# Kernel optimization log

Measured on AMD Instinct MI355X. Metric: run time of the kernel, lower is better.

The kernel has to match this reference:

```python
import jax, jax.numpy as jnp
import numpy as np

NHEAD = 8
K_NEIGH = 16


def setup_inputs() -> dict:
    key = jax.random.key(0)
    ks = jax.random.split(key, 6)
    B, L, D = 4, 4096, 512
    x = jax.random.normal(ks[0], (B, L, D), dtype=jnp.float32)
    positions = jax.random.uniform(ks[1], (B, L, 3), dtype=jnp.float32)
    in_proj_w = jax.random.normal(ks[2], (3 * D, D), dtype=jnp.float32) * 0.02
    in_proj_b = jax.random.normal(ks[3], (3 * D,), dtype=jnp.float32) * 0.02
    out_proj_w = jax.random.normal(ks[4], (D, D), dtype=jnp.float32) * 0.02
    out_proj_b = jax.random.normal(ks[5], (D,), dtype=jnp.float32) * 0.02
    return {"x": x, "positions": positions, "in_proj_w": in_proj_w,
            "in_proj_b": in_proj_b, "out_proj_w": out_proj_w, "out_proj_b": out_proj_b}


def _sparse_attention(x, positions, in_proj_w, in_proj_b, out_proj_w, out_proj_b):
    B, L, D = x.shape
    H, dh = NHEAD, D // NHEAD
    K = min(K_NEIGH, L)
    scale = 1.0 / jnp.sqrt(jnp.asarray(dh, x.dtype))

    # Pairwise distances [B, L, L]; topk smallest -> neighbor indices [B, L, K].
    diff = positions[:, :, None, :] - positions[:, None, :, :]
    dist = jnp.sqrt(jnp.sum(diff * diff, axis=-1))
    _, nbr = jax.lax.top_k(-dist, K)  # [B, L, K]

    Wq, Wk, Wv = in_proj_w[:D], in_proj_w[D:2 * D], in_proj_w[2 * D:]
    bq, bk, bv = in_proj_b[:D], in_proj_b[D:2 * D], in_proj_b[2 * D:]

    # Query is x[b, i] itself (self is always its own nearest neighbor at dist 0),
    # so the selected attention row equals attention with query x[b, i] over neighbors.
    q = ((x @ Wq.T + bq) * scale).reshape(B, L, H, dh)

    # Gather neighbor features: [B, L, K, D]
    b_idx = jnp.arange(B)[:, None, None]
    local_x = x[b_idx, nbr]
    k = (local_x @ Wk.T + bk).reshape(B, L, K, H, dh)
    v = (local_x @ Wv.T + bv).reshape(B, L, K, H, dh)

    scores = jnp.einsum('blhd,blkhd->blhk', q, k)
    attn = jax.nn.softmax(scores, axis=-1)
    ctx = jnp.einsum('blhk,blkhd->blhd', attn, v).reshape(B, L, D)
    out = ctx @ out_proj_w.T + out_proj_b

    # Faithful fallback: if i not among its neighbors, pass through x[b, i].
    is_in = jnp.any(nbr == jnp.arange(L)[None, :, None], axis=-1)  # [B, L]
    return jnp.where(is_in[..., None], out, x)


def reference(x, positions, in_proj_w, in_proj_b, out_proj_w, out_proj_b):
    return _sparse_attention(x, positions, in_proj_w, in_proj_b, out_proj_w, out_proj_b)
```

## Files before the change

### kernel.cpp

```cpp
#include <hip/hip_runtime.h>
#include <cfloat>
#include <cmath>

constexpr int B = 4;
constexpr int L = 4096;
constexpr int D = 512;
constexpr int NH = 8;
constexpr int DH = 64;
constexpr int KN = 16;
constexpr int M = B * L;
constexpr int N_IN = 3 * D;
constexpr int NCELL = 512;

typedef __attribute__((ext_vector_type(8))) short short8;
typedef __attribute__((ext_vector_type(4))) float f32x4;
typedef unsigned short ushort;

__device__ __forceinline__ ushort f2bf(float f) {
  unsigned u = __float_as_uint(f);
  u = u + 0x7fffu + ((u >> 16) & 1u);
  return (ushort)(u >> 16);
}
__device__ __forceinline__ float bf2f(ushort h) {
  return __uint_as_float(((unsigned)h) << 16);
}
__device__ __forceinline__ float dot8(const uint4 qu, const uint4 ku, float a) {
  a = fmaf(bf2f((ushort)qu.x), bf2f((ushort)ku.x), a);
  a = fmaf(bf2f((ushort)(qu.x >> 16)), bf2f((ushort)(ku.x >> 16)), a);
  a = fmaf(bf2f((ushort)qu.y), bf2f((ushort)ku.y), a);
  a = fmaf(bf2f((ushort)(qu.y >> 16)), bf2f((ushort)(ku.y >> 16)), a);
  a = fmaf(bf2f((ushort)qu.z), bf2f((ushort)ku.z), a);
  a = fmaf(bf2f((ushort)(qu.z >> 16)), bf2f((ushort)(ku.z >> 16)), a);
  a = fmaf(bf2f((ushort)qu.w), bf2f((ushort)ku.w), a);
  a = fmaf(bf2f((ushort)(qu.w >> 16)), bf2f((ushort)(ku.w >> 16)), a);
  return a;
}
__device__ __forceinline__ void acc8(float wgt, const uint4 vv, float (&acc)[8]) {
  acc[0] = fmaf(wgt, bf2f((ushort)vv.x), acc[0]);
  acc[1] = fmaf(wgt, bf2f((ushort)(vv.x >> 16)), acc[1]);
  acc[2] = fmaf(wgt, bf2f((ushort)vv.y), acc[2]);
  acc[3] = fmaf(wgt, bf2f((ushort)(vv.y >> 16)), acc[3]);
  acc[4] = fmaf(wgt, bf2f((ushort)vv.z), acc[4]);
  acc[5] = fmaf(wgt, bf2f((ushort)(vv.z >> 16)), acc[5]);
  acc[6] = fmaf(wgt, bf2f((ushort)vv.w), acc[6]);
  acc[7] = fmaf(wgt, bf2f((ushort)(vv.w >> 16)), acc[7]);
}
__device__ __forceinline__ uint2 pack4hi(const float4 v) {
  uint2 o;
  o.x = (unsigned)f2bf(v.x) | ((unsigned)f2bf(v.y) << 16);
  o.y = (unsigned)f2bf(v.z) | ((unsigned)f2bf(v.w) << 16);
  return o;
}
__device__ __forceinline__ void gload16(const void* g, void* l) {
  __builtin_amdgcn_global_load_lds(
      (const __attribute__((address_space(1))) void*)g,
      (__attribute__((address_space(3))) void*)l, 16, 0, 0);
}
__device__ __forceinline__ int morton3(int x, int y, int z) {
  int m = 0;
#pragma unroll
  for (int i = 0; i < 3; ++i)
    m |= (((x >> i) & 1) << (3 * i + 2)) | (((y >> i) & 1) << (3 * i + 1)) |
         (((z >> i) & 1) << (3 * i));
  return m;
}

__global__ __launch_bounds__(256) void cvt_x_kernel(const float* __restrict__ in,
                                                    ushort* __restrict__ out) {
  const int n8 = M * D / 8;
  for (int i = blockIdx.x * 256 + threadIdx.x; i < n8; i += gridDim.x * 256) {
    const float4 v0 = reinterpret_cast<const float4*>(in)[i * 2];
    const float4 v1 = reinterpret_cast<const float4*>(in)[i * 2 + 1];
    uint4 o;
    const uint2 a = pack4hi(v0), b2 = pack4hi(v1);
    o.x = a.x; o.y = a.y; o.z = b2.x; o.w = b2.y;
    reinterpret_cast<uint4*>(out)[i] = o;
  }
}

__global__ __launch_bounds__(256) void cvt_w_kernel(const float* __restrict__ in_w,
                                                    const float* __restrict__ out_w,
                                                    ushort* __restrict__ iwh,
                                                    ushort* __restrict__ owh,
                                                    ushort* __restrict__ owl) {
  const int ni8 = N_IN * D / 8;
  const int no8 = D * D / 8;
  for (int i = blockIdx.x * 256 + threadIdx.x; i < ni8 + no8; i += gridDim.x * 256) {
    if (i < ni8) {
      const float4 v0 = reinterpret_cast<const float4*>(in_w)[i * 2];
      const float4 v1 = reinterpret_cast<const float4*>(in_w)[i * 2 + 1];
      uint4 o;
      const uint2 a = pack4hi(v0), b2 = pack4hi(v1);
      o.x = a.x; o.y = a.y; o.z = b2.x; o.w = b2.y;
      reinterpret_cast<uint4*>(iwh)[i] = o;
    } else {
      const int j = i - ni8;
      const float4 v0 = reinterpret_cast<const float4*>(out_w)[j * 2];
      const float4 v1 = reinterpret_cast<const float4*>(out_w)[j * 2 + 1];
      uint4 oh, ol;
      const uint2 a = pack4hi(v0), b2 = pack4hi(v1);
      oh.x = a.x; oh.y = a.y; oh.z = b2.x; oh.w = b2.y;
      const float4 r0 = make_float4(v0.x - bf2f(f2bf(v0.x)), v0.y - bf2f(f2bf(v0.y)),
                                    v0.z - bf2f(f2bf(v0.z)), v0.w - bf2f(f2bf(v0.w)));
      const float4 r1 = make_float4(v1.x - bf2f(f2bf(v1.x)), v1.y - bf2f(f2bf(v1.y)),
                                    v1.z - bf2f(f2bf(v1.z)), v1.w - bf2f(f2bf(v1.w)));
      const uint2 c = pack4hi(r0), d2 = pack4hi(r1);
      ol.x = c.x; ol.y = c.y; ol.z = d2.x; ol.w = d2.y;
      reinterpret_cast<uint4*>(owh)[j] = oh;
      reinterpret_cast<uint4*>(owl)[j] = ol;
    }
  }
}

__global__ __launch_bounds__(512) void sort_kernel(const float* __restrict__ pos,
                                                   int* __restrict__ qorder) {
  __shared__ int hist[NCELL];
  __shared__ int scanbuf[NCELL];
  const int b = blockIdx.x;
  const int t = threadIdx.x;
  hist[t] = 0;
  __syncthreads();

  int cells[8], ranks[8];
  const float* p = pos + (size_t)b * L * 3;
#pragma unroll
  for (int q = 0; q < 8; ++q) {
    const int i = q * 512 + t;
    const int ix = min(7, max(0, (int)(p[3 * i + 0] * 8.f)));
    const int iy = min(7, max(0, (int)(p[3 * i + 1] * 8.f)));
    const int iz = min(7, max(0, (int)(p[3 * i + 2] * 8.f)));
    cells[q] = morton3(ix, iy, iz);
    ranks[q] = atomicAdd(&hist[cells[q]], 1);
  }
  __syncthreads();

  int accv = hist[t];
  const int orig = accv;
  scanbuf[t] = accv;
  __syncthreads();
  for (int s = 1; s < NCELL; s <<= 1) {
    const int o = (t >= s) ? scanbuf[t - s] : 0;
    __syncthreads();
    accv += o;
    scanbuf[t] = accv;
    __syncthreads();
  }
  hist[t] = accv - orig;
  __syncthreads();

#pragma unroll
  for (int q = 0; q < 8; ++q) {
    const int i = q * 512 + t;
    qorder[b * L + hist[cells[q]] + ranks[q]] = i;
  }
}

constexpr int TP = 65;

__global__ __launch_bounds__(512) void topk_kernel(const float* __restrict__ pos,
                                                   int* __restrict__ nbr,
                                                   int* __restrict__ isin) {
  __shared__ float sxT[64 * TP], syT[64 * TP], szT[64 * TP];
  __shared__ unsigned long long lst[8 * 64];
  const int wave = threadIdx.x >> 6;
  const int lane = threadIdx.x & 63;
  const int b = blockIdx.x >> 9;
  const int l = (blockIdx.x & 511) * 8 + wave;
  const int row = b * L + l;

  const float* p = pos + (size_t)b * L * 3;
  for (int i = threadIdx.x; i < L; i += 512) {
    const int a = (i & 63) * TP + (i >> 6);
    sxT[a] = p[3 * i + 0];
    syT[a] = p[3 * i + 1];
    szT[a] = p[3 * i + 2];
  }
  __syncthreads();

  const int qa = (l & 63) * TP + (l >> 6);
  const float qx = sxT[qa], qy = syT[qa], qz = szT[qa];

  float mA = FLT_MAX, mB2 = FLT_MAX, mC = FLT_MAX, mD2 = FLT_MAX;
  const int base = lane * TP;
  for (int j = 0; j < 64; j += 4) {
#define D2(t, acc)                                                   \
    {                                                                \
      const int a = base + j + t;                                    \
      const float dx = qx - sxT[a], dy = qy - syT[a], dz = qz - szT[a]; \
      acc = fminf(acc, fmaf(dx, dx, fmaf(dy, dy, dz * dz)));         \
    }
    D2(0, mA) D2(1, mB2) D2(2, mC) D2(3, mD2)
#undef D2
  }
  const unsigned mbits = __float_as_uint(fminf(fminf(mA, mB2), fminf(mC, mD2)));

  unsigned lo = 1, hi = 0x40400001u;
  while (lo < hi) {
    const unsigned mid = (lo + hi) >> 1;
    const int c = __popcll(__ballot(mbits < mid));
    if (c >= 16) hi = mid; else lo = mid + 1;
  }
  const unsigned P = lo + 16;

  int cnt = 0;
  unsigned long long am = __ballot(mbits < P);
  const unsigned long long below = (1ull << lane) - 1ull;
  while (am) {
    const int pl = (int)__builtin_ctzll(am);
    am &= am - 1;
    const int a = pl * TP + lane;
    const float dx = qx - sxT[a], dy = qy - syT[a], dz = qz - szT[a];
    const float d2 = fmaf(dx, dx, fmaf(dy, dy, dz * dz));
    const bool hit = __float_as_uint(d2) < P;
    const unsigned long long msk = __ballot(hit);
    if (hit) {
      const int slot = cnt + __popcll(msk & below);
      if (slot < 64) {
        const unsigned c = (unsigned)(lane * 64 + pl);
        lst[wave * 64 + slot] =
            ((unsigned long long)__float_as_uint(sqrtf(d2)) << 32) | c;
      }
    }
    cnt += __popcll(msk);
  }
  const int n = min(cnt, 64);

  const unsigned long long mine = (lane < n) ? lst[wave * 64 + lane] : ~0ull;
  int r = 0;
  for (int i = 0; i < n; ++i) r += (lst[wave * 64 + i] < mine) ? 1 : 0;

  const int idx = (int)(unsigned)(mine & 0xffffffffu);
  const bool wr = (lane < n) && (r < 16);
  if (wr) nbr[(size_t)row * KN + r] = idx;
  const unsigned long long hit2 = __ballot(wr && idx == l);
  if (lane == 0) isin[row] = hit2 ? 1 : 0;
}

constexpr int BM = 128, BN = 128, BK = 32;
constexpr int BK2 = 64;

__global__ __launch_bounds__(256) void gemm_in(const ushort* __restrict__ A,
                                               const ushort* __restrict__ W,
                                               const float* __restrict__ bias,
                                               ushort* __restrict__ qb,
                                               ushort* __restrict__ kb,
                                               ushort* __restrict__ vb) {
  __shared__ ushort Ah[BM * BK2];
  __shared__ ushort Bh[BN * BK2];

  const int tid = threadIdx.x;
  const int m0 = blockIdx.x * BM;
  const int n0 = blockIdx.y * BN;

  const int wv = tid >> 6;
  const int lane = tid & 63;
  const int srow0 = wv * 8 + (lane >> 3);
  const int gchunk = (lane & 7) ^ (lane >> 3);
  const ushort* Asrc = A + (size_t)(m0 + srow0) * D + gchunk * 8;
  const ushort* Wsrc = W + (size_t)(n0 + srow0) * D + gchunk * 8;
  ushort* AhB0 = Ah + (wv * 8) * BK2;
  ushort* AhB1 = Ah + (wv * 8 + 32) * BK2;
  ushort* AhB2 = Ah + (wv * 8 + 64) * BK2;
  ushort* AhB3 = Ah + (wv * 8 + 96) * BK2;
  ushort* BhB0 = Bh + (wv * 8) * BK2;
  ushort* BhB1 = Bh + (wv * 8 + 32) * BK2;
  ushort* BhB2 = Bh + (wv * 8 + 64) * BK2;
  ushort* BhB3 = Bh + (wv * 8 + 96) * BK2;

  const int wr0 = (wv >> 1) * 64;
  const int wc0 = (wv & 1) * 64;
  const int fr_row = lane & 15;
  const int cbase = lane >> 4;
  const int rx = lane & 7;

  f32x4 acc[4][4];
#pragma unroll
  for (int i = 0; i < 4; ++i)
#pragma unroll
    for (int j = 0; j < 4; ++j) acc[i][j] = {0.f, 0.f, 0.f, 0.f};

  for (int k0 = 0; k0 < D; k0 += BK2) {
    __syncthreads();
    gload16(Asrc + k0, AhB0);
    gload16(Asrc + (size_t)32 * D + k0, AhB1);
    gload16(Asrc + (size_t)64 * D + k0, AhB2);
    gload16(Asrc + (size_t)96 * D + k0, AhB3);
    gload16(Wsrc + k0, BhB0);
    gload16(Wsrc + (size_t)32 * D + k0, BhB1);
    gload16(Wsrc + (size_t)64 * D + k0, BhB2);
    gload16(Wsrc + (size_t)96 * D + k0, BhB3);
    __syncthreads();

#pragma unroll
    for (int kk = 0; kk < 2; ++kk) {
      const int slot = (kk * 4 + cbase) ^ rx;
      short8 ah[4];
#pragma unroll
      for (int fr = 0; fr < 4; ++fr)
        ah[fr] = *reinterpret_cast<const short8*>(
            &Ah[(wr0 + fr * 16 + fr_row) * BK2 + slot * 8]);
#pragma unroll
      for (int fc = 0; fc < 4; ++fc) {
        const short8 bh = *reinterpret_cast<const short8*>(
            &Bh[(wc0 + fc * 16 + fr_row) * BK2 + slot * 8]);
#pragma unroll
        for (int fr = 0; fr < 4; ++fr)
          acc[fr][fc] = __builtin_amdgcn_mfma_f32_16x16x32_bf16(ah[fr], bh, acc[fr][fc], 0, 0, 0);
      }
    }
  }

  const int region = n0 >> 9;
  ushort* outb = region == 0 ? qb : (region == 1 ? kb : vb);
  const float scl = region == 0 ? 0.125f : 1.0f;
  const int nloc0 = (n0 & 511) + wc0;
#pragma unroll
  for (int fr = 0; fr < 4; ++fr) {
#pragma unroll
    for (int r = 0; r < 4; ++r) {
      const int grow = m0 + wr0 + fr * 16 + (lane >> 4) * 4 + r;
#pragma unroll
      for (int fc = 0; fc < 4; ++fc) {
        const int cc = fc * 16 + (lane & 15);
        const float v = (acc[fr][fc][r] + bias[n0 + wc0 + cc]) * scl;
        outb[(size_t)grow * D + nloc0 + cc] = f2bf(v);
      }
    }
  }
}

__global__ __launch_bounds__(256) void gemm_out(const ushort* __restrict__ A,
                                                const ushort* __restrict__ Wh,
                                                const ushort* __restrict__ Wl,
                                                const float* __restrict__ bias,
                                                float* __restrict__ C,
                                                const float* __restrict__ X,
                                                const int* __restrict__ isin) {
  __shared__ ushort Ah[BM * BK];
  __shared__ ushort Bh[BN * BK];
  __shared__ ushort Bl[BN * BK];

  const int tid = threadIdx.x;
  const int m0 = blockIdx.x * BM;
  const int n0 = blockIdx.y * BN;

  const int wv = tid >> 6;
  const int lane = tid & 63;
  const int sr = wv * 16 + (lane >> 2);
  const int sc = (lane & 3) * 8;
  const ushort* Asrc = A + (size_t)(m0 + sr) * D + sc;
  const ushort* Hsrc = Wh + (size_t)(n0 + sr) * D + sc;
  const ushort* Lsrc = Wl + (size_t)(n0 + sr) * D + sc;
  ushort* AhB0 = Ah + (wv * 16) * BK;
  ushort* AhB1 = Ah + (wv * 16 + 64) * BK;
  ushort* BhB0 = Bh + (wv * 16) * BK;
  ushort* BhB1 = Bh + (wv * 16 + 64) * BK;
  ushort* BlB0 = Bl + (wv * 16) * BK;
  ushort* BlB1 = Bl + (wv * 16 + 64) * BK;

  const int wr0 = (wv >> 1) * 64;
  const int wc0 = (wv & 1) * 64;
  const int fr_row = lane & 15;
  const int kof = (lane >> 4) * 8;

  f32x4 acc[4][4];
#pragma unroll
  for (int i = 0; i < 4; ++i)
#pragma unroll
    for (int j = 0; j < 4; ++j) acc[i][j] = {0.f, 0.f, 0.f, 0.f};

  for (int k0 = 0; k0 < D; k0 += BK) {
    __syncthreads();
    gload16(Asrc + k0, AhB0);
    gload16(Asrc + (size_t)64 * D + k0, AhB1);
    gload16(Hsrc + k0, BhB0);
    gload16(Hsrc + (size_t)64 * D + k0, BhB1);
    gload16(Lsrc + k0, BlB0);
    gload16(Lsrc + (size_t)64 * D + k0, BlB1);
    __syncthreads();

    short8 ah[4];
#pragma unroll
    for (int fr = 0; fr < 4; ++fr)
      ah[fr] = *reinterpret_cast<const short8*>(&Ah[(wr0 + fr * 16 + fr_row) * BK + kof]);
#pragma unroll
    for (int fc = 0; fc < 4; ++fc) {
      const short8 bh = *reinterpret_cast<const short8*>(&Bh[(wc0 + fc * 16 + fr_row) * BK + kof]);
      const short8 bl = *reinterpret_cast<const short8*>(&Bl[(wc0 + fc * 16 + fr_row) * BK + kof]);
#pragma unroll
      for (int fr = 0; fr < 4; ++fr) {
        acc[fr][fc] = __builtin_amdgcn_mfma_f32_16x16x32_bf16(ah[fr], bh, acc[fr][fc], 0, 0, 0);
        acc[fr][fc] = __builtin_amdgcn_mfma_f32_16x16x32_bf16(ah[fr], bl, acc[fr][fc], 0, 0, 0);
      }
    }
  }

#pragma unroll
  for (int fr = 0; fr < 4; ++fr) {
#pragma unroll
    for (int r = 0; r < 4; ++r) {
      const int grow = m0 + wr0 + fr * 16 + (lane >> 4) * 4 + r;
      const int ok = isin[grow];
#pragma unroll
      for (int fc = 0; fc < 4; ++fc) {
        const int gcol = n0 + wc0 + fc * 16 + (lane & 15);
        float v = acc[fr][fc][r] + bias[gcol];
        if (!ok) v = X[(size_t)grow * D + gcol];
        C[(size_t)grow * D + gcol] = v;
      }
    }
  }
}

__global__ __launch_bounds__(256) void attn_kernel(const ushort* __restrict__ qb,
                                                   const ushort* __restrict__ kb,
                                                   const ushort* __restrict__ vb,
                                                   const int* __restrict__ nbr,
                                                   const int* __restrict__ qorder,
                                                   ushort* __restrict__ ctx) {
  const int wave = threadIdx.x >> 6;
  const int lane = threadIdx.x & 63;
  const int xcd = blockIdx.x & 7;
  const int chunk = blockIdx.x >> 3;
  const int b = xcd >> 1;
  const int slot = ((xcd & 1) * 512 + chunk) * 4 + wave;
  const int l = qorder[b * L + slot];
  const int bl = b * L + l;
  const int bbase = b * L;
  const int* nb = nbr + (size_t)bl * KN;

  const int h = lane >> 3;
  const int n0 = lane & 7;
  const int glane = h * 8;

  const ushort* qp = qb + (size_t)bl * D + h * DH;
  uint4 qv[8];
#pragma unroll
  for (int i = 0; i < 8; ++i)
    qv[i] = *reinterpret_cast<const uint4*>(qp + i * 8);

  const int j0 = nb[n0];
  const int j1 = nb[n0 + 8];
  float a0 = 0.f, a1 = 0.f;
  {
    const ushort* kr0 = kb + (size_t)(bbase + j0) * D + h * DH;
    const ushort* kr1 = kb + (size_t)(bbase + j1) * D + h * DH;
#pragma unroll
    for (int i = 0; i < 8; ++i) {
      a0 = dot8(qv[i], *reinterpret_cast<const uint4*>(kr0 + i * 8), a0);
      a1 = dot8(qv[i], *reinterpret_cast<const uint4*>(kr1 + i * 8), a1);
    }
  }

  float mx = fmaxf(a0, a1);
  mx = fmaxf(mx, __shfl_xor(mx, 1));
  mx = fmaxf(mx, __shfl_xor(mx, 2));
  mx = fmaxf(mx, __shfl_xor(mx, 4));
  const float e0 = expf(a0 - mx), e1 = expf(a1 - mx);
  float sm = e0 + e1;
  sm += __shfl_xor(sm, 1);
  sm += __shfl_xor(sm, 2);
  sm += __shfl_xor(sm, 4);
  const float inv = 1.0f / sm;
  const float w0 = e0 * inv, w1 = e1 * inv;

  float ww[KN];
  int jj[KN];
#pragma unroll
  for (int n = 0; n < KN; ++n) {
    const int src = glane + (n & 7);
    ww[n] = __shfl((n < 8) ? w0 : w1, src);
    jj[n] = __shfl((n < 8) ? j0 : j1, src);
  }

  const int d0 = n0 * 8;
  const ushort* vbase = vb + (size_t)bbase * D + h * DH + d0;
  float acc[8];
#pragma unroll
  for (int i = 0; i < 8; ++i) acc[i] = 0.f;

#pragma unroll
  for (int g = 0; g < KN; g += 4) {
    const uint4 va0 = *reinterpret_cast<const uint4*>(vbase + (size_t)jj[g] * D);
    const uint4 va1 = *reinterpret_cast<const uint4*>(vbase + (size_t)jj[g + 1] * D);
    const uint4 va2 = *reinterpret_cast<const uint4*>(vbase + (size_t)jj[g + 2] * D);
    const uint4 va3 = *reinterpret_cast<const uint4*>(vbase + (size_t)jj[g + 3] * D);
    acc8(ww[g], va0, acc);
    acc8(ww[g + 1], va1, acc);
    acc8(ww[g + 2], va2, acc);
    acc8(ww[g + 3], va3, acc);
  }

  uint4 o;
  o.x = (unsigned)f2bf(acc[0]) | ((unsigned)f2bf(acc[1]) << 16);
  o.y = (unsigned)f2bf(acc[2]) | ((unsigned)f2bf(acc[3]) << 16);
  o.z = (unsigned)f2bf(acc[4]) | ((unsigned)f2bf(acc[5]) << 16);
  o.w = (unsigned)f2bf(acc[6]) | ((unsigned)f2bf(acc[7]) << 16);
  *reinterpret_cast<uint4*>(ctx + (size_t)bl * D + h * DH + d0) = o;
}

extern "C" void kernel_launch(void* const* d_in, const int* in_sizes, int n_in,
                              void* d_out, int out_size, void* d_ws, size_t ws_size,
                              hipStream_t stream) {
  const float* x     = (const float*)d_in[0];
  const float* pos   = (const float*)d_in[1];
  const float* in_w  = (const float*)d_in[2];
  const float* in_b  = (const float*)d_in[3];
  const float* out_w = (const float*)d_in[4];
  const float* out_b = (const float*)d_in[5];
  float* out = (float*)d_out;

  const size_t nbr_bytes  = (size_t)M * KN * sizeof(int);
  const size_t isin_bytes = (size_t)M * sizeof(int);
  const size_t half_bytes = (size_t)M * D * sizeof(ushort);
  const size_t iwh_bytes  = (size_t)N_IN * D * sizeof(ushort);
  const size_t ow_bytes   = (size_t)D * D * sizeof(ushort);
  const size_t sort_bytes = (size_t)M * sizeof(int);
  const size_t need = nbr_bytes + isin_bytes + 5 * half_bytes +
                      iwh_bytes + 2 * ow_bytes + sort_bytes + 16384;
  if (ws_size < need) return;

  char* w = (char*)d_ws;
  int*    nbr    = (int*)w;    w += (nbr_bytes + 255) & ~(size_t)255;
  int*    isin   = (int*)w;    w += (isin_bytes + 255) & ~(size_t)255;
  ushort* xb     = (ushort*)w; w += (half_bytes + 255) & ~(size_t)255;
  ushort* qb     = (ushort*)w; w += (half_bytes + 255) & ~(size_t)255;
  ushort* kb     = (ushort*)w; w += (half_bytes + 255) & ~(size_t)255;
  ushort* vb     = (ushort*)w; w += (half_bytes + 255) & ~(size_t)255;
  ushort* ctxb   = (ushort*)w; w += (half_bytes + 255) & ~(size_t)255;
  ushort* iwh    = (ushort*)w; w += (iwh_bytes + 255) & ~(size_t)255;
  ushort* owh    = (ushort*)w; w += (ow_bytes + 255) & ~(size_t)255;
  ushort* owl    = (ushort*)w; w += (ow_bytes + 255) & ~(size_t)255;
  int*    qorder = (int*)w;

  cvt_x_kernel<<<2048, 256, 0, stream>>>(x, xb);
  cvt_w_kernel<<<512, 256, 0, stream>>>(in_w, out_w, iwh, owh, owl);

  sort_kernel<<<B, 512, 0, stream>>>(pos, qorder);

  topk_kernel<<<B * (L / 8), 512, 0, stream>>>(pos, nbr, isin);

  gemm_in<<<dim3(M / BM, N_IN / BN), 256, 0, stream>>>(xb, iwh, in_b, qb, kb, vb);

  attn_kernel<<<M / 4, 256, 0, stream>>>(qb, kb, vb, nbr, qorder, ctxb);

  gemm_out<<<dim3(M / BM, D / BN), 256, 0, stream>>>(ctxb, owh, owl, out_b, out, x, isin);
}
```

Before: 166.3 us.

## Merge preprocessing kernels into one launch and widen gemm_out K-tile with swizzle

Combines the x conversion, weight conversion, Morton sort and top-k neighbor kernels into a single heterogeneous launch that dispatches on block index, so the independent stages can run concurrently and fewer launches are issued. gemm_out also moves from a 32-wide K tile to a 64-wide one with an XOR-swizzled LDS layout, which halves the K-loop iterations and barriers and is meant to avoid LDS bank conflicts. In exchange, every stage0 block reserves the shared memory of all branches, which may lower occupancy for the top-k blocks, and gemm_out uses a larger LDS footprint.

```diff
diff --git a/kernel.cpp b/kernel.cpp
--- a/kernel.cpp
+++ b/kernel.cpp
@@ -65,178 +65,185 @@
   return m;
 }
 
-__global__ __launch_bounds__(256) void cvt_x_kernel(const float* __restrict__ in,
-                                                    ushort* __restrict__ out) {
-  const int n8 = M * D / 8;
-  for (int i = blockIdx.x * 256 + threadIdx.x; i < n8; i += gridDim.x * 256) {
-    const float4 v0 = reinterpret_cast<const float4*>(in)[i * 2];
-    const float4 v1 = reinterpret_cast<const float4*>(in)[i * 2 + 1];
-    uint4 o;
-    const uint2 a = pack4hi(v0), b2 = pack4hi(v1);
-    o.x = a.x; o.y = a.y; o.z = b2.x; o.w = b2.y;
-    reinterpret_cast<uint4*>(out)[i] = o;
-  }
-}
-
-__global__ __launch_bounds__(256) void cvt_w_kernel(const float* __restrict__ in_w,
-                                                    const float* __restrict__ out_w,
-                                                    ushort* __restrict__ iwh,
-                                                    ushort* __restrict__ owh,
-                                                    ushort* __restrict__ owl) {
-  const int ni8 = N_IN * D / 8;
-  const int no8 = D * D / 8;
-  for (int i = blockIdx.x * 256 + threadIdx.x; i < ni8 + no8; i += gridDim.x * 256) {
-    if (i < ni8) {
-      const float4 v0 = reinterpret_cast<const float4*>(in_w)[i * 2];
-      const float4 v1 = reinterpret_cast<const float4*>(in_w)[i * 2 + 1];
+constexpr int TP = 65;
+constexpr int TOPK_BLKS = B * (L / 8);
+constexpr int SORT_BLKS = B;
+constexpr int CVTX_BLKS = 1024;
+constexpr int CVTW_BLKS = 256;
+constexpr int STAGE0_BLKS = TOPK_BLKS + SORT_BLKS + CVTX_BLKS + CVTW_BLKS;
+
+__global__ __launch_bounds__(512) void stage0_kernel(
+    const float* __restrict__ pos, const float* __restrict__ x,
+    const float* __restrict__ in_w, const float* __restrict__ out_w,
+    int* __restrict__ nbr, int* __restrict__ isin, int* __restrict__ qorder,
+    ushort* __restrict__ xb, ushort* __restrict__ iwh,
+    ushort* __restrict__ owh, ushort* __restrict__ owl) {
+  __shared__ float sxT[64 * TP], syT[64 * TP], szT[64 * TP];
+  __shared__ unsigned long long lst[8 * 64];
+  __shared__ int hist[NCELL];
+  __shared__ int scanbuf[NCELL];
+
+  const int bid = blockIdx.x;
+  const int tid = threadIdx.x;
+
+  if (bid < TOPK_BLKS) {
+    const int wave = tid >> 6;
+    const int lane = tid & 63;
+    const int b = bid >> 9;
+    const int l = (bid & 511) * 8 + wave;
+    const int row = b * L + l;
+
+    const float* p = pos + (size_t)b * L * 3;
+    for (int i = tid; i < L; i += 512) {
+      const int a = (i & 63) * TP + (i >> 6);
+      sxT[a] = p[3 * i + 0];
+      syT[a] = p[3 * i + 1];
+      szT[a] = p[3 * i + 2];
+    }
+    __syncthreads();
+
+    const int qa = (l & 63) * TP + (l >> 6);
+    const float qx = sxT[qa], qy = syT[qa], qz = szT[qa];
+
+    float mA = FLT_MAX, mB2 = FLT_MAX, mC = FLT_MAX, mD2 = FLT_MAX;
+    const int base = lane * TP;
+    for (int j = 0; j < 64; j += 4) {
+#define D2(t, acc)                                                   \
+      {                                                              \
+        const int a = base + j + t;                                  \
+        const float dx = qx - sxT[a], dy = qy - syT[a], dz = qz - szT[a]; \
+        acc = fminf(acc, fmaf(dx, dx, fmaf(dy, dy, dz * dz)));       \
+      }
+      D2(0, mA) D2(1, mB2) D2(2, mC) D2(3, mD2)
+#undef D2
+    }
+    const unsigned mbits = __float_as_uint(fminf(fminf(mA, mB2), fminf(mC, mD2)));
+
+    unsigned lo = 1, hi = 0x40400001u;
+    while (lo < hi) {
+      const unsigned mid = (lo + hi) >> 1;
+      const int c = __popcll(__ballot(mbits < mid));
+      if (c >= 16) hi = mid; else lo = mid + 1;
+    }
+    const unsigned P = lo + 16;
+
+    int cnt = 0;
+    unsigned long long am = __ballot(mbits < P);
+    const unsigned long long below = (1ull << lane) - 1ull;
+    while (am) {
+      const int pl = (int)__builtin_ctzll(am);
+      am &= am - 1;
+      const int a = pl * TP + lane;
+      const float dx = qx - sxT[a], dy = qy - syT[a], dz = qz - szT[a];
+      const float d2 = fmaf(dx, dx, fmaf(dy, dy, dz * dz));
+      const bool hit = __float_as_uint(d2) < P;
+      const unsigned long long msk = __ballot(hit);
+      if (hit) {
+        const int slot = cnt + __popcll(msk & below);
+        if (slot < 64) {
+          const unsigned c = (unsigned)(lane * 64 + pl);
+          lst[wave * 64 + slot] =
+              ((unsigned long long)__float_as_uint(sqrtf(d2)) << 32) | c;
+        }
+      }
+      cnt += __popcll(msk);
+    }
+    const int n = min(cnt, 64);
+
+    const unsigned long long mine = (lane < n) ? lst[wave * 64 + lane] : ~0ull;
+    int r = 0;
+    for (int i = 0; i < n; ++i) r += (lst[wave * 64 + i] < mine) ? 1 : 0;
+
+    const int idx = (int)(unsigned)(mine & 0xffffffffu);
+    const bool wr = (lane < n) && (r < 16);
+    if (wr) nbr[(size_t)row * KN + r] = idx;
+    const unsigned long long hit2 = __ballot(wr && idx == l);
+    if (lane == 0) isin[row] = hit2 ? 1 : 0;
+
+  } else if (bid < TOPK_BLKS + SORT_BLKS) {
+    const int b = bid - TOPK_BLKS;
+    const int t = tid;
+    hist[t] = 0;
+    __syncthreads();
+
+    int cells[8], ranks[8];
+    const float* p = pos + (size_t)b * L * 3;
+#pragma unroll
+    for (int q = 0; q < 8; ++q) {
+      const int i = q * 512 + t;
+      const int ix = min(7, max(0, (int)(p[3 * i + 0] * 8.f)));
+      const int iy = min(7, max(0, (int)(p[3 * i + 1] * 8.f)));
+      const int iz = min(7, max(0, (int)(p[3 * i + 2] * 8.f)));
+      cells[q] = morton3(ix, iy, iz);
+      ranks[q] = atomicAdd(&hist[cells[q]], 1);
+    }
+    __syncthreads();
+
+    int accv = hist[t];
+    const int orig = accv;
+    scanbuf[t] = accv;
+    __syncthreads();
+    for (int s = 1; s < NCELL; s <<= 1) {
+      const int o = (t >= s) ? scanbuf[t - s] : 0;
+      __syncthreads();
+      accv += o;
+      scanbuf[t] = accv;
+      __syncthreads();
+    }
+    hist[t] = accv - orig;
+    __syncthreads();
+
+#pragma unroll
+    for (int q = 0; q < 8; ++q) {
+      const int i = q * 512 + t;
+      qorder[b * L + hist[cells[q]] + ranks[q]] = i;
+    }
+
+  } else if (bid < TOPK_BLKS + SORT_BLKS + CVTX_BLKS) {
+    const int vb = bid - TOPK_BLKS - SORT_BLKS;
+    const int n8 = M * D / 8;
+    for (int i = vb * 512 + tid; i < n8; i += CVTX_BLKS * 512) {
+      const float4 v0 = reinterpret_cast<const float4*>(x)[i * 2];
+      const float4 v1 = reinterpret_cast<const float4*>(x)[i * 2 + 1];
       uint4 o;
       const uint2 a = pack4hi(v0), b2 = pack4hi(v1);
       o.x = a.x; o.y = a.y; o.z = b2.x; o.w = b2.y;
-      reinterpret_cast<uint4*>(iwh)[i] = o;
-    } else {
-      const int j = i - ni8;
-      const float4 v0 = reinterpret_cast<const float4*>(out_w)[j * 2];
-      const float4 v1 = reinterpret_cast<const float4*>(out_w)[j * 2 + 1];
-      uint4 oh, ol;
-      const uint2 a = pack4hi(v0), b2 = pack4hi(v1);
-      oh.x = a.x; oh.y = a.y; oh.z = b2.x; oh.w = b2.y;
-      const float4 r0 = make_float4(v0.x - bf2f(f2bf(v0.x)), v0.y - bf2f(f2bf(v0.y)),
-                                    v0.z - bf2f(f2bf(v0.z)), v0.w - bf2f(f2bf(v0.w)));
-      const float4 r1 = make_float4(v1.x - bf2f(f2bf(v1.x)), v1.y - bf2f(f2bf(v1.y)),
-                                    v1.z - bf2f(f2bf(v1.z)), v1.w - bf2f(f2bf(v1.w)));
-      const uint2 c = pack4hi(r0), d2 = pack4hi(r1);
-      ol.x = c.x; ol.y = c.y; ol.z = d2.x; ol.w = d2.y;
-      reinterpret_cast<uint4*>(owh)[j] = oh;
-      reinterpret_cast<uint4*>(owl)[j] = ol;
-    }
-  }
-}
-
-__global__ __launch_bounds__(512) void sort_kernel(const float* __restrict__ pos,
-                                                   int* __restrict__ qorder) {
-  __shared__ int hist[NCELL];
-  __shared__ int scanbuf[NCELL];
-  const int b = blockIdx.x;
-  const int t = threadIdx.x;
-  hist[t] = 0;
-  __syncthreads();
-
-  int cells[8], ranks[8];
-  const float* p = pos + (size_t)b * L * 3;
-#pragma unroll
-  for (int q = 0; q < 8; ++q) {
-    const int i = q * 512 + t;
-    const int ix = min(7, max(0, (int)(p[3 * i + 0] * 8.f)));
-    const int iy = min(7, max(0, (int)(p[3 * i + 1] * 8.f)));
-    const int iz = min(7, max(0, (int)(p[3 * i + 2] * 8.f)));
-    cells[q] = morton3(ix, iy, iz);
-    ranks[q] = atomicAdd(&hist[cells[q]], 1);
-  }
-  __syncthreads();
-
-  int accv = hist[t];
-  const int orig = accv;
-  scanbuf[t] = accv;
-  __syncthreads();
-  for (int s = 1; s < NCELL; s <<= 1) {
-    const int o = (t >= s) ? scanbuf[t - s] : 0;
-    __syncthreads();
-    accv += o;
-    scanbuf[t] = accv;
-    __syncthreads();
-  }
-  hist[t] = accv - orig;
-  __syncthreads();
-
-#pragma unroll
-  for (int q = 0; q < 8; ++q) {
-    const int i = q * 512 + t;
-    qorder[b * L + hist[cells[q]] + ranks[q]] = i;
-  }
-}
-
-constexpr int TP = 65;
-
-__global__ __launch_bounds__(512) void topk_kernel(const float* __restrict__ pos,
-                                                   int* __restrict__ nbr,
-                                                   int* __restrict__ isin) {
-  __shared__ float sxT[64 * TP], syT[64 * TP], szT[64 * TP];
-  __shared__ unsigned long long lst[8 * 64];
-  const int wave = threadIdx.x >> 6;
-  const int lane = threadIdx.x & 63;
-  const int b = blockIdx.x >> 9;
-  const int l = (blockIdx.x & 511) * 8 + wave;
-  const int row = b * L + l;
-
-  const float* p = pos + (size_t)b * L * 3;
-  for (int i = threadIdx.x; i < L; i += 512) {
-    const int a = (i & 63) * TP + (i >> 6);
-    sxT[a] = p[3 * i + 0];
-    syT[a] = p[3 * i + 1];
-    szT[a] = p[3 * i + 2];
-  }
-  __syncthreads();
-
-  const int qa = (l & 63) * TP + (l >> 6);
-  const float qx = sxT[qa], qy = syT[qa], qz = szT[qa];
-
-  float mA = FLT_MAX, mB2 = FLT_MAX, mC = FLT_MAX, mD2 = FLT_MAX;
-  const int base = lane * TP;
-  for (int j = 0; j < 64; j += 4) {
-#define D2(t, acc)                                                   \
-    {                                                                \
-      const int a = base + j + t;                                    \
-      const float dx = qx - sxT[a], dy = qy - syT[a], dz = qz - szT[a]; \
-      acc = fminf(acc, fmaf(dx, dx, fmaf(dy, dy, dz * dz)));         \
-    }
-    D2(0, mA) D2(1, mB2) D2(2, mC) D2(3, mD2)
-#undef D2
-  }
-  const unsigned mbits = __float_as_uint(fminf(fminf(mA, mB2), fminf(mC, mD2)));
-
-  unsigned lo = 1, hi = 0x40400001u;
-  while (lo < hi) {
-    const unsigned mid = (lo + hi) >> 1;
-    const int c = __popcll(__ballot(mbits < mid));
-    if (c >= 16) hi = mid; else lo = mid + 1;
-  }
-  const unsigned P = lo + 16;
-
-  int cnt = 0;
-  unsigned long long am = __ballot(mbits < P);
-  const unsigned long long below = (1ull << lane) - 1ull;
-  while (am) {
-    const int pl = (int)__builtin_ctzll(am);
-    am &= am - 1;
-    const int a = pl * TP + lane;
-    const float dx = qx - sxT[a], dy = qy - syT[a], dz = qz - szT[a];
-    const float d2 = fmaf(dx, dx, fmaf(dy, dy, dz * dz));
-    const bool hit = __float_as_uint(d2) < P;
-    const unsigned long long msk = __ballot(hit);
-    if (hit) {
-      const int slot = cnt + __popcll(msk & below);
-      if (slot < 64) {
-        const unsigned c = (unsigned)(lane * 64 + pl);
-        lst[wave * 64 + slot] =
-            ((unsigned long long)__float_as_uint(sqrtf(d2)) << 32) | c;
-      }
-    }
-    cnt += __popcll(msk);
-  }
-  const int n = min(cnt, 64);
-
-  const unsigned long long mine = (lane < n) ? lst[wave * 64 + lane] : ~0ull;
-  int r = 0;
-  for (int i = 0; i < n; ++i) r += (lst[wave * 64 + i] < mine) ? 1 : 0;
-
-  const int idx = (int)(unsigned)(mine & 0xffffffffu);
-  const bool wr = (lane < n) && (r < 16);
-  if (wr) nbr[(size_t)row * KN + r] = idx;
-  const unsigned long long hit2 = __ballot(wr && idx == l);
-  if (lane == 0) isin[row] = hit2 ? 1 : 0;
-}
-
-constexpr int BM = 128, BN = 128, BK = 32;
+      reinterpret_cast<uint4*>(xb)[i] = o;
+    }
+
+  } else {
+    const int vb = bid - TOPK_BLKS - SORT_BLKS - CVTX_BLKS;
+    const int ni8 = N_IN * D / 8;
+    const int no8 = D * D / 8;
+    for (int i = vb * 512 + tid; i < ni8 + no8; i += CVTW_BLKS * 512) {
+      if (i < ni8) {
+        const float4 v0 = reinterpret_cast<const float4*>(in_w)[i * 2];
+        const float4 v1 = reinterpret_cast<const float4*>(in_w)[i * 2 + 1];
+        uint4 o;
+        const uint2 a = pack4hi(v0), b2 = pack4hi(v1);
+        o.x = a.x; o.y = a.y; o.z = b2.x; o.w = b2.y;
+        reinterpret_cast<uint4*>(iwh)[i] = o;
+      } else {
+        const int j = i - ni8;
+        const float4 v0 = reinterpret_cast<const float4*>(out_w)[j * 2];
+        const float4 v1 = reinterpret_cast<const float4*>(out_w)[j * 2 + 1];
+        uint4 oh, ol;
+        const uint2 a = pack4hi(v0), b2 = pack4hi(v1);
+        oh.x = a.x; oh.y = a.y; oh.z = b2.x; oh.w = b2.y;
+        const float4 r0 = make_float4(v0.x - bf2f(f2bf(v0.x)), v0.y - bf2f(f2bf(v0.y)),
+                                      v0.z - bf2f(f2bf(v0.z)), v0.w - bf2f(f2bf(v0.w)));
+        const float4 r1 = make_float4(v1.x - bf2f(f2bf(v1.x)), v1.y - bf2f(f2bf(v1.y)),
+                                      v1.z - bf2f(f2bf(v1.z)), v1.w - bf2f(f2bf(v1.w)));
+        const uint2 c = pack4hi(r0), d2 = pack4hi(r1);
+        ol.x = c.x; ol.y = c.y; ol.z = d2.x; ol.w = d2.y;
+        reinterpret_cast<uint4*>(owh)[j] = oh;
+        reinterpret_cast<uint4*>(owl)[j] = ol;
+      }
+    }
+  }
+}
+
+constexpr int BM = 128, BN = 128;
 constexpr int BK2 = 64;
 
 __global__ __launch_bounds__(256) void gemm_in(const ushort* __restrict__ A,
@@ -336,9 +343,9 @@
                                                 float* __restrict__ C,
                                                 const float* __restrict__ X,
                                                 const int* __restrict__ isin) {
-  __shared__ ushort Ah[BM * BK];
-  __shared__ ushort Bh[BN * BK];
-  __shared__ ushort Bl[BN * BK];
+  __shared__ ushort Ah[BM * BK2];
+  __shared__ ushort Bh[BN * BK2];
+  __shared__ ushort Bl[BN * BK2];
 
   const int tid = threadIdx.x;
   const int m0 = blockIdx.x * BM;
@@ -346,22 +353,29 @@
 
   const int wv = tid >> 6;
   const int lane = tid & 63;
-  const int sr = wv * 16 + (lane >> 2);
-  const int sc = (lane & 3) * 8;
-  const ushort* Asrc = A + (size_t)(m0 + sr) * D + sc;
-  const ushort* Hsrc = Wh + (size_t)(n0 + sr) * D + sc;
-  const ushort* Lsrc = Wl + (size_t)(n0 + sr) * D + sc;
-  ushort* AhB0 = Ah + (wv * 16) * BK;
-  ushort* AhB1 = Ah + (wv * 16 + 64) * BK;
-  ushort* BhB0 = Bh + (wv * 16) * BK;
-  ushort* BhB1 = Bh + (wv * 16 + 64) * BK;
-  ushort* BlB0 = Bl + (wv * 16) * BK;
-  ushort* BlB1 = Bl + (wv * 16 + 64) * BK;
+  const int srow0 = wv * 8 + (lane >> 3);
+  const int gchunk = (lane & 7) ^ (lane >> 3);
+  const ushort* Asrc = A + (size_t)(m0 + srow0) * D + gchunk * 8;
+  const ushort* Hsrc = Wh + (size_t)(n0 + srow0) * D + gchunk * 8;
+  const ushort* Lsrc = Wl + (size_t)(n0 + srow0) * D + gchunk * 8;
+  ushort* AhB0 = Ah + (wv * 8) * BK2;
+  ushort* AhB1 = Ah + (wv * 8 + 32) * BK2;
+  ushort* AhB2 = Ah + (wv * 8 + 64) * BK2;
+  ushort* AhB3 = Ah + (wv * 8 + 96) * BK2;
+  ushort* BhB0 = Bh + (wv * 8) * BK2;
+  ushort* BhB1 = Bh + (wv * 8 + 32) * BK2;
+  ushort* BhB2 = Bh + (wv * 8 + 64) * BK2;
+  ushort* BhB3 = Bh + (wv * 8 + 96) * BK2;
+  ushort* BlB0 = Bl + (wv * 8) * BK2;
+  ushort* BlB1 = Bl + (wv * 8 + 32) * BK2;
+  ushort* BlB2 = Bl + (wv * 8 + 64) * BK2;
+  ushort* BlB3 = Bl + (wv * 8 + 96) * BK2;
 
   const int wr0 = (wv >> 1) * 64;
   const int wc0 = (wv & 1) * 64;
   const int fr_row = lane & 15;
-  const int kof = (lane >> 4) * 8;
+  const int cbase = lane >> 4;
+  const int rx = lane & 7;
 
   f32x4 acc[4][4];
 #pragma unroll
@@ -369,28 +383,41 @@
 #pragma unroll
     for (int j = 0; j < 4; ++j) acc[i][j] = {0.f, 0.f, 0.f, 0.f};
 
-  for (int k0 = 0; k0 < D; k0 += BK) {
+  for (int k0 = 0; k0 < D; k0 += BK2) {
     __syncthreads();
     gload16(Asrc + k0, AhB0);
-    gload16(Asrc + (size_t)64 * D + k0, AhB1);
+    gload16(Asrc + (size_t)32 * D + k0, AhB1);
+    gload16(Asrc + (size_t)64 * D + k0, AhB2);
+    gload16(Asrc + (size_t)96 * D + k0, AhB3);
     gload16(Hsrc + k0, BhB0);
-    gload16(Hsrc + (size_t)64 * D + k0, BhB1);
+    gload16(Hsrc + (size_t)32 * D + k0, BhB1);
+    gload16(Hsrc + (size_t)64 * D + k0, BhB2);
+    gload16(Hsrc + (size_t)96 * D + k0, BhB3);
     gload16(Lsrc + k0, BlB0);
-    gload16(Lsrc + (size_t)64 * D + k0, BlB1);
-    __syncthreads();
-
-    short8 ah[4];
-#pragma unroll
-    for (int fr = 0; fr < 4; ++fr)
-      ah[fr] = *reinterpret_cast<const short8*>(&Ah[(wr0 + fr * 16 + fr_row) * BK + kof]);
-#pragma unroll
-    for (int fc = 0; fc < 4; ++fc) {
-      const short8 bh = *reinterpret_cast<const short8*>(&Bh[(wc0 + fc * 16 + fr_row) * BK + kof]);
-      const short8 bl = *reinterpret_cast<const short8*>(&Bl[(wc0 + fc * 16 + fr_row) * BK + kof]);
-#pragma unroll
-      for (int fr = 0; fr < 4; ++fr) {
-        acc[fr][fc] = __builtin_amdgcn_mfma_f32_16x16x32_bf16(ah[fr], bh, acc[fr][fc], 0, 0, 0);
-        acc[fr][fc] = __builtin_amdgcn_mfma_f32_16x16x32_bf16(ah[fr], bl, acc[fr][fc], 0, 0, 0);
+    gload16(Lsrc + (size_t)32 * D + k0, BlB1);
+    gload16(Lsrc + (size_t)64 * D + k0, BlB2);
+    gload16(Lsrc + (size_t)96 * D + k0, BlB3);
+    __syncthreads();
+
+#pragma unroll
+    for (int kk = 0; kk < 2; ++kk) {
+      const int slot = (kk * 4 + cbase) ^ rx;
+      short8 ah[4];
+#pragma unroll
+      for (int fr = 0; fr < 4; ++fr)
+        ah[fr] = *reinterpret_cast<const short8*>(
+            &Ah[(wr0 + fr * 16 + fr_row) * BK2 + slot * 8]);
+#pragma unroll
+      for (int fc = 0; fc < 4; ++fc) {
+        const short8 bh = *reinterpret_cast<const short8*>(
+            &Bh[(wc0 + fc * 16 + fr_row) * BK2 + slot * 8]);
+        const short8 bl = *reinterpret_cast<const short8*>(
+            &Bl[(wc0 + fc * 16 + fr_row) * BK2 + slot * 8]);
+#pragma unroll
+        for (int fr = 0; fr < 4; ++fr) {
+          acc[fr][fc] = __builtin_amdgcn_mfma_f32_16x16x32_bf16(ah[fr], bh, acc[fr][fc], 0, 0, 0);
+          acc[fr][fc] = __builtin_amdgcn_mfma_f32_16x16x32_bf16(ah[fr], bl, acc[fr][fc], 0, 0, 0);
+        }
       }
     }
   }
@@ -533,12 +560,8 @@
   ushort* owl    = (ushort*)w; w += (ow_bytes + 255) & ~(size_t)255;
   int*    qorder = (int*)w;
 
-  cvt_x_kernel<<<2048, 256, 0, stream>>>(x, xb);
-  cvt_w_kernel<<<512, 256, 0, stream>>>(in_w, out_w, iwh, owh, owl);
-
-  sort_kernel<<<B, 512, 0, stream>>>(pos, qorder);
-
-  topk_kernel<<<B * (L / 8), 512, 0, stream>>>(pos, nbr, isin);
+  stage0_kernel<<<STAGE0_BLKS, 512, 0, stream>>>(
+      pos, x, in_w, out_w, nbr, isin, qorder, xb, iwh, owh, owl);
 
   gemm_in<<<dim3(M / BM, N_IN / BN), 256, 0, stream>>>(xb, iwh, in_b, qb, kb, vb);
 
```

After: 150.5 us. -9.5%, faster.
